# Optimization experiments

Hardware: AMD Instinct MI355X
Metric: run time of the kernel (lower is better)

Reference implementation:

```python
import jax, jax.numpy as jnp
import numpy as np


def _layernorm(x, g, b, eps=1e-5):
    m = x.mean(-1, keepdims=True)
    v = ((x - m) ** 2).mean(-1, keepdims=True)
    return (x - m) / jnp.sqrt(v + eps) * g + b


def _rotate_every_two(x):
    x1 = x[..., ::2]
    x2 = x[..., 1::2]
    return jnp.stack([-x2, x1], axis=-1).reshape(x.shape)


def _segsum(x):
    # x: (..., L) of negative decay rates -> (..., L, L) bidirectional segment sums
    cs = jnp.cumsum(x, axis=-1)
    d = cs[..., :, None] - cs[..., None, :]
    L = x.shape[-1]
    i = jnp.arange(L)[:, None]
    j = jnp.arange(L)[None, :]
    # lower-tri (incl diag): cs[i]-cs[j]; strict upper: cs[j]-cs[i]; diag is 0
    return jnp.where(i >= j, d, -d)


def _forward(x, y, th, dw1_w, dw1_b, dw2_w, dw2_b, qw, qb, kw, kb, vw, vb,
             lepe_w, lepe_b, dt_w, dt_bias, A_log, ow, ob,
             n1_g, n1_b, ffn_w1, ffn_b1, ffn_w2, ffn_b2, n2_g, n2_b):
    B, C, H, W = x.shape
    nh = dt_bias.shape[0]
    hd = C // nh
    scaling = hd ** (-0.5)

    # dynamic gated fusion of the two kv branches (1x1 convs == channel matmuls)
    fusion = jnp.concatenate([y, th], axis=1)                      # (B,2C,H,W)
    hid = jax.nn.relu(jnp.einsum('bchw,oc->bohw', fusion, dw1_w) + dw1_b[None, :, None, None])
    logits = jnp.einsum('bchw,oc->bohw', hid, dw2_w) + dw2_b[None, :, None, None]
    wts = jax.nn.softmax(logits, axis=1)                           # (B,2,H,W)
    fused = y * wts[:, 0:1] + th * wts[:, 1:2]

    xh = jnp.transpose(x, (0, 2, 3, 1))                            # (B,H,W,C)
    fkv = jnp.transpose(fused, (0, 2, 3, 1))

    # 2D RoPE tables (flattened raster index)
    angle = jnp.repeat(1.0 / 10000 ** jnp.linspace(0.0, 1.0, hd // 2), 2)
    idx = jnp.arange(H * W, dtype=x.dtype)
    sin = jnp.sin(idx[:, None] * angle[None, :]).reshape(H, W, hd)
    cos = jnp.cos(idx[:, None] * angle[None, :]).reshape(H, W, hd)

    q = xh @ qw + qb
    k = fkv @ kw + kb
    v = fkv @ vw + vb

    # depthwise 5x5 conv position term on v (NHWC)
    lepe = jax.lax.conv_general_dilated(
        v, lepe_w, (1, 1), ((2, 2), (2, 2)),
        dimension_numbers=('NHWC', 'HWIO', 'NHWC'), feature_group_count=C) + lepe_b

    k = k * scaling
    q = q.reshape(B, H, W, nh, hd).transpose(0, 3, 1, 2, 4)        # (B,nh,H,W,hd)
    k = k.reshape(B, H, W, nh, hd).transpose(0, 3, 1, 2, 4)
    v5 = v.reshape(B, H, W, nh, hd).transpose(0, 3, 1, 2, 4)

    qr = q * cos + _rotate_every_two(q) * sin
    kr = k * cos + _rotate_every_two(k) * sin

    # PathEmbeding2D: data-dependent decay masks
    xt = xh.reshape(B, H * W, nh, hd)
    dt = xt @ dt_w                                                 # (B,S,nh,2)
    A = -jnp.exp(A_log)                                            # (nh,)
    da = jax.nn.softplus(dt[..., 0] + dt_bias) * A                 # (B,S,nh)
    db = jax.nn.softplus(dt[..., 1] + dt_bias) * A
    mask_w = _segsum(da.reshape(B, H, W, nh).transpose(0, 1, 3, 2))  # (B,H,nh,W,W)
    mask_h = _segsum(db.reshape(B, H, W, nh).transpose(0, 2, 3, 1))  # (B,W,nh,H,H)

    # row (width-direction) and column (height-direction) attentions
    qk_w = jax.nn.softmax(jnp.einsum('bnhid,bnhjd->bhnij', qr, kr) + mask_w, axis=-1)  # (B,H,nh,W,W)
    qk_h = jax.nn.softmax(jnp.einsum('bnhwd,bngwd->bwnhg', qr, kr) + mask_h, axis=-1)  # (B,W,nh,H,H)

    v_w = jnp.einsum('bhnij,bnhjd->bhnid', qk_w, v5)               # (B,H,nh,W,hd)
    out1 = jnp.einsum('bwnhg,bgnwd->bwnhd', qk_h, v_w)             # (B,W,nh,H,hd)
    out1 = out1.transpose(0, 3, 1, 2, 4).reshape(B, H, W, C)

    v_h = jnp.einsum('bwnhg,bngwd->bwnhd', qk_h, v5)               # (B,W,nh,H,hd)
    out2 = jnp.einsum('bhnij,bjnhd->bhnid', qk_w, v_h)             # (B,H,nh,W,hd)
    out2 = out2.transpose(0, 1, 3, 2, 4).reshape(B, H, W, C)

    out = 0.5 * out1 + 0.5 * out2 + lepe
    out = out @ ow + ob
    out = _layernorm(xh + out, n1_g, n1_b)
    ffn = jax.nn.gelu(out @ ffn_w1 + ffn_b1, approximate=False) @ ffn_w2 + ffn_b2
    out = _layernorm(out + ffn, n2_g, n2_b)
    return jnp.transpose(out, (0, 3, 1, 2))                        # (B,C,H,W)


def setup_inputs() -> dict:
    B, C, H, W, nh = 4, 64, 128, 128, 4
    hd = C // nh
    key = jax.random.key(0)
    ks = jax.random.split(key, 20)
    n = lambda k, shp, s: jax.random.normal(k, shp, dtype=jnp.float32) * s
    rng = np.random.default_rng(0)
    dt = np.exp(rng.uniform(0.0, 1.0, nh) * (np.log(0.1) - np.log(0.001)) + np.log(0.001))
    dt = np.clip(dt, 1e-4, None)
    dt_bias = jnp.asarray(dt + np.log(-np.expm1(-dt)), dtype=jnp.float32)
    A_log = jnp.asarray(np.log(rng.uniform(1.0, 1.1, nh)), dtype=jnp.float32)
    inp = {
        'x': n(ks[0], (B, C, H, W), 1.0),
        'y': n(ks[1], (B, C, H, W), 1.0),
        'th': n(ks[2], (B, C, H, W), 1.0),
        'dw1_w': n(ks[3], (C, 2 * C), (2 * C) ** -0.5),
        'dw1_b': jnp.zeros((C,), jnp.float32),
        'dw2_w': n(ks[4], (2, C), C ** -0.5),
        'dw2_b': jnp.zeros((2,), jnp.float32),
        'qw': n(ks[5], (C, C), 0.2 * C ** -0.5),
        'qb': jnp.zeros((C,), jnp.float32),
        'kw': n(ks[6], (C, C), 0.2 * C ** -0.5),
        'kb': jnp.zeros((C,), jnp.float32),
        'vw': n(ks[7], (C, C), 0.2 * C ** -0.5),
        'vb': jnp.zeros((C,), jnp.float32),
        'lepe_w': n(ks[8], (5, 5, 1, C), 0.1),
        'lepe_b': jnp.zeros((C,), jnp.float32),
        'dt_w': n(ks[9], (hd, 2), hd ** -0.5),
        'dt_bias': dt_bias,
        'A_log': A_log,
        'ow': n(ks[10], (C, C), C ** -0.5),
        'ob': jnp.zeros((C,), jnp.float32),
        'n1_g': jnp.ones((C,), jnp.float32),
        'n1_b': jnp.zeros((C,), jnp.float32),
        'ffn_w1': n(ks[11], (C, 4 * C), C ** -0.5),
        'ffn_b1': jnp.zeros((4 * C,), jnp.float32),
        'ffn_w2': n(ks[12], (4 * C, C), (4 * C) ** -0.5),
        'ffn_b2': jnp.zeros((C,), jnp.float32),
        'n2_g': jnp.ones((C,), jnp.float32),
        'n2_b': jnp.zeros((C,), jnp.float32),
    }
    return inp


def reference(x, y, th, dw1_w, dw1_b, dw2_w, dw2_b, qw, qb, kw, kb, vw, vb,
              lepe_w, lepe_b, dt_w, dt_bias, A_log, ow, ob,
              n1_g, n1_b, ffn_w1, ffn_b1, ffn_w2, ffn_b2, n2_g, n2_b):
    return _forward(x, y, th, dw1_w, dw1_b, dw2_w, dw2_b, qw, qb, kw, kb, vw, vb,
                    lepe_w, lepe_b, dt_w, dt_bias, A_log, ow, ob,
                    n1_g, n1_b, ffn_w1, ffn_b1, ffn_w2, ffn_b2, n2_g, n2_b)
```

## Files before the change

### kernel.cpp

```cpp
#include <hip/hip_runtime.h>
#include <math.h>

#define HWSZ 16384

typedef __attribute__((ext_vector_type(8))) short bf16x8;
typedef __attribute__((ext_vector_type(4))) float f32x4;

__device__ __forceinline__ float gelu_f(float v) {
    return 0.5f * v * (1.0f + erff(v * 0.70710678118654752f));
}
__device__ __forceinline__ float splus_f(float v) {
    return (v > 20.f) ? v : log1pf(expf(v));
}
__device__ __forceinline__ unsigned short f2bf(float f) {
    union { float f; unsigned u; } v; v.f = f;
    unsigned r = (v.u + 0x7FFF + ((v.u >> 16) & 1)) >> 16;
    return (unsigned short)r;
}
__device__ __forceinline__ unsigned pk2(float a, float b) {
    return (unsigned)f2bf(a) | ((unsigned)f2bf(b) << 16);
}
__device__ __forceinline__ float bf2f(unsigned short s) {
    union { unsigned u; float f; } v; v.u = ((unsigned)s) << 16; return v.f;
}

#define W1S 68
__global__ __launch_bounds__(256) void k_fuse(
    const float* __restrict__ y, const float* __restrict__ th,
    const float* __restrict__ w1, const float* __restrict__ b1,
    const float* __restrict__ w2, const float* __restrict__ b2,
    float* __restrict__ fused)
{
    __shared__ unsigned short fsh[8192];
    __shared__ float w1t[128*W1S];
    int tid = threadIdx.x;
    int g = blockIdx.x;
    int b = g >> 8;
    int p0 = (g & 255)*64;
    for (int i = tid; i < 8192; i += 256) {
        int o = i >> 7, c = i & 127;
        w1t[c*W1S + o] = w1[i];
    }
    for (int vi = tid; vi < 1024; vi += 256) {
        int c = vi >> 4, p4 = (vi & 15)*4;
        float4 yv = *(const float4*)&y [((size_t)(b*64+c))*HWSZ + p0 + p4];
        float4 tv = *(const float4*)&th[((size_t)(b*64+c))*HWSZ + p0 + p4];
        *(uint2*)&fsh[c*64 + p4]      = make_uint2(pk2(yv.x,yv.y), pk2(yv.z,yv.w));
        *(uint2*)&fsh[(64+c)*64 + p4] = make_uint2(pk2(tv.x,tv.y), pk2(tv.z,tv.w));
    }
    __syncthreads();
    int lane = tid & 63, wv = tid >> 6;
    int po = lane & 15, oc = lane >> 4;
    int pos = wv*16 + po;
    float acc[16];
    #pragma unroll
    for (int d4 = 0; d4 < 4; ++d4) {
        float4 bv = *(const float4*)&b1[oc*16 + d4*4];
        acc[d4*4+0]=bv.x; acc[d4*4+1]=bv.y; acc[d4*4+2]=bv.z; acc[d4*4+3]=bv.w;
    }
    for (int c = 0; c < 128; ++c) {
        float xc = bf2f(fsh[c*64 + pos]);
        #pragma unroll
        for (int d4 = 0; d4 < 4; ++d4) {
            float4 wv4 = *(const float4*)&w1t[c*W1S + oc*16 + d4*4];
            acc[d4*4+0] += wv4.x*xc; acc[d4*4+1] += wv4.y*xc;
            acc[d4*4+2] += wv4.z*xc; acc[d4*4+3] += wv4.w*xc;
        }
    }
    float l0 = 0.f, l1 = 0.f;
    #pragma unroll
    for (int d4 = 0; d4 < 4; ++d4) {
        float4 wa4 = *(const float4*)&w2[oc*16 + d4*4];
        float4 wb4 = *(const float4*)&w2[64 + oc*16 + d4*4];
        float h0 = fmaxf(acc[d4*4+0],0.f), h1 = fmaxf(acc[d4*4+1],0.f);
        float h2 = fmaxf(acc[d4*4+2],0.f), h3 = fmaxf(acc[d4*4+3],0.f);
        l0 += wa4.x*h0 + wa4.y*h1 + wa4.z*h2 + wa4.w*h3;
        l1 += wb4.x*h0 + wb4.y*h1 + wb4.z*h2 + wb4.w*h3;
    }
    l0 += __shfl_xor(l0, 16, 64); l0 += __shfl_xor(l0, 32, 64);
    l1 += __shfl_xor(l1, 16, 64); l1 += __shfl_xor(l1, 32, 64);
    l0 += b2[0]; l1 += b2[1];
    float m = fmaxf(l0, l1);
    float e0 = __expf(l0 - m), e1 = __expf(l1 - m);
    float inv = 1.f/(e0 + e1);
    float wa = e0*inv, wb = e1*inv;
    float* fb = fused + (size_t)b*64*HWSZ + p0 + pos;
    #pragma unroll
    for (int u = 0; u < 16; ++u) {
        int c = oc*16 + u;
        float fv = bf2f(fsh[c*64 + pos])*wa + bf2f(fsh[(64+c)*64 + pos])*wb;
        fb[(size_t)c*HWSZ] = fv;
    }
}

__global__ __launch_bounds__(256) void k_qkv(
    const float* __restrict__ x, const float* __restrict__ fused,
    const float* __restrict__ qw, const float* __restrict__ qb,
    const float* __restrict__ kw, const float* __restrict__ kb,
    const float* __restrict__ vw, const float* __restrict__ vb,
    const float* __restrict__ dtw, const float* __restrict__ dtb,
    const float* __restrict__ alog,
    float* __restrict__ qr, float* __restrict__ kr, float* __restrict__ v5,
    float* __restrict__ da, float* __restrict__ db)
{
    __shared__ float sw[12288];
    __shared__ float sx[4096];
    int tid = threadIdx.x;
    for (int i = tid*4; i < 4096; i += 1024) {
        *(float4*)&sw[i]      = *(const float4*)&qw[i];
        *(float4*)&sw[4096+i] = *(const float4*)&kw[i];
        *(float4*)&sw[8192+i] = *(const float4*)&vw[i];
    }
    int b  = blockIdx.x >> 8;
    int p0 = (blockIdx.x & 255)*64;
    for (int vi = tid; vi < 1024; vi += 256) {
        int c = vi >> 4, p4 = (vi & 15)*4;
        *(float4*)&sx[c*64 + p4] = *(const float4*)&x[((size_t)(b*64+c))*HWSZ + p0 + p4];
    }
    __syncthreads();
    int lane = tid & 63;
    int n = tid >> 6;
    int p = p0 + lane;
    int h = p >> 7, w = p & 127;
    float sn[8], cn[8];
    #pragma unroll
    for (int t = 0; t < 8; ++t) {
        float ang = exp2f(-1.89824462565f * (float)t);
        sincosf((float)p * ang, &sn[t], &cn[t]);
    }
    float a[16];
    #pragma unroll
    for (int d = 0; d < 16; ++d) a[d] = qb[n*16+d];
    for (int c = 0; c < 64; ++c) {
        float xc = sx[c*64 + lane];
        #pragma unroll
        for (int d4 = 0; d4 < 4; ++d4) {
            float4 wv = *(const float4*)&sw[c*64 + n*16 + d4*4];
            a[d4*4+0] += wv.x*xc; a[d4*4+1] += wv.y*xc;
            a[d4*4+2] += wv.z*xc; a[d4*4+3] += wv.w*xc;
        }
    }
    {
        float r[16];
        #pragma unroll
        for (int t = 0; t < 8; ++t) {
            r[2*t]   = a[2*t]*cn[t]   - a[2*t+1]*sn[t];
            r[2*t+1] = a[2*t+1]*cn[t] + a[2*t]*sn[t];
        }
        float* dst = qr + (((size_t)(b*4+n))*HWSZ + p)*16;
        #pragma unroll
        for (int d4 = 0; d4 < 4; ++d4)
            *(float4*)&dst[d4*4] = make_float4(r[d4*4],r[d4*4+1],r[d4*4+2],r[d4*4+3]);
    }
    {
        float dt0 = 0.f, dt1 = 0.f;
        #pragma unroll
        for (int d = 0; d < 16; ++d) {
            float xv = sx[(n*16+d)*64 + lane];
            dt0 += xv*dtw[2*d];
            dt1 += xv*dtw[2*d+1];
        }
        float A  = -expf(alog[n]);
        float bb = dtb[n];
        da[((b*128+h)*4+n)*128 + w] = splus_f(dt0+bb)*A;
        db[((b*128+w)*4+n)*128 + h] = splus_f(dt1+bb)*A;
    }
    __syncthreads();
    for (int vi = tid; vi < 1024; vi += 256) {
        int c = vi >> 4, p4 = (vi & 15)*4;
        *(float4*)&sx[c*64 + p4] = *(const float4*)&fused[((size_t)(b*64+c))*HWSZ + p0 + p4];
    }
    __syncthreads();
    #pragma unroll
    for (int d = 0; d < 16; ++d) a[d] = kb[n*16+d];
    for (int c = 0; c < 64; ++c) {
        float xc = sx[c*64 + lane];
        #pragma unroll
        for (int d4 = 0; d4 < 4; ++d4) {
            float4 wv = *(const float4*)&sw[4096 + c*64 + n*16 + d4*4];
            a[d4*4+0] += wv.x*xc; a[d4*4+1] += wv.y*xc;
            a[d4*4+2] += wv.z*xc; a[d4*4+3] += wv.w*xc;
        }
    }
    {
        float r[16];
        #pragma unroll
        for (int t = 0; t < 8; ++t) {
            float e = a[2*t]*0.25f, o = a[2*t+1]*0.25f;
            r[2*t]   = e*cn[t] - o*sn[t];
            r[2*t+1] = o*cn[t] + e*sn[t];
        }
        float* dst = kr + (((size_t)(b*4+n))*HWSZ + p)*16;
        #pragma unroll
        for (int d4 = 0; d4 < 4; ++d4)
            *(float4*)&dst[d4*4] = make_float4(r[d4*4],r[d4*4+1],r[d4*4+2],r[d4*4+3]);
    }
    #pragma unroll
    for (int d = 0; d < 16; ++d) a[d] = vb[n*16+d];
    for (int c = 0; c < 64; ++c) {
        float xc = sx[c*64 + lane];
        #pragma unroll
        for (int d4 = 0; d4 < 4; ++d4) {
            float4 wv = *(const float4*)&sw[8192 + c*64 + n*16 + d4*4];
            a[d4*4+0] += wv.x*xc; a[d4*4+1] += wv.y*xc;
            a[d4*4+2] += wv.z*xc; a[d4*4+3] += wv.w*xc;
        }
    }
    {
        float* dst = v5 + (((size_t)(b*4+n))*HWSZ + p)*16;
        #pragma unroll
        for (int d4 = 0; d4 < 4; ++d4)
            *(float4*)&dst[d4*4] = make_float4(a[d4*4],a[d4*4+1],a[d4*4+2],a[d4*4+3]);
    }
}

__global__ __launch_bounds__(256) void k_cumsum(float* __restrict__ da, float* __restrict__ db)
{
    int gw = (blockIdx.x*256 + threadIdx.x) >> 6;
    int lane = threadIdx.x & 63;
    float* base = (gw < 2048) ? (da + (size_t)gw*128) : (db + (size_t)(gw-2048)*128);
    float2 e = *(float2*)&base[lane*2];
    float s = e.x + e.y;
    #pragma unroll
    for (int d = 1; d < 64; d <<= 1) {
        float t = __shfl_up(s, d, 64);
        if (lane >= d) s += t;
    }
    float excl = s - (e.x + e.y);
    float2 o;
    o.x = excl + e.x;
    o.y = excl + e.x + e.y;
    *(float2*)&base[lane*2] = o;
}

#define LROW 328
__global__ __launch_bounds__(256) void k_lepe(
    const float* __restrict__ v5, const float* __restrict__ lw,
    const float* __restrict__ lb, float* __restrict__ lepe)
{
    __shared__ float sv[36*LROW];
    __shared__ float swt[400];
    int tid = threadIdx.x, bid = blockIdx.x;
    int tw = bid & 7, th_ = (bid >> 3) & 3, n = (bid >> 5) & 3, b = bid >> 7;
    int bn = b*4 + n;
    int h0 = th_*32, w0 = tw*16;
    for (int i = tid; i < 400; i += 256) {
        int tap = i >> 4, d = i & 15;
        swt[i] = lw[tap*64 + n*16 + d];
    }
    const float* vb = v5 + (size_t)bn*HWSZ*16;
    for (int vi = tid; vi < 2880; vi += 256) {
        int hh = vi / 80;
        int rem = vi - hh*80;
        int ww = rem >> 2, df = (rem & 3)*4;
        int h = h0 - 2 + hh, w = w0 - 2 + ww;
        float4 val = make_float4(0.f,0.f,0.f,0.f);
        if (h >= 0 && h < 128 && w >= 0 && w < 128)
            val = *(const float4*)&vb[((size_t)(h*128+w))*16 + df];
        *(float4*)&sv[hh*LROW + ww*16 + df] = val;
    }
    __syncthreads();
    int df = (tid & 3)*4;
    int s  = tid >> 2;
    int ph = s >> 1;
    int pw = (s & 1)*8;
    float4 bv = *(const float4*)&lb[n*16 + df];
    float acc[8][4];
    #pragma unroll
    for (int ow = 0; ow < 8; ++ow) {
        acc[ow][0] = bv.x; acc[ow][1] = bv.y; acc[ow][2] = bv.z; acc[ow][3] = bv.w;
    }
    #pragma unroll
    for (int ky = 0; ky < 5; ++ky) {
        float wgt[5][4];
        #pragma unroll
        for (int kx = 0; kx < 5; ++kx) {
            float4 wv = *(const float4*)&swt[(ky*5+kx)*16 + df];
            wgt[kx][0]=wv.x; wgt[kx][1]=wv.y; wgt[kx][2]=wv.z; wgt[kx][3]=wv.w;
        }
        float dat[13][4];
        #pragma unroll
        for (int c = 0; c < 13; ++c) {
            float4 dv = *(const float4*)&sv[(ph+ky)*LROW + (pw+c)*16 + df];
            dat[c][0]=dv.x; dat[c][1]=dv.y; dat[c][2]=dv.z; dat[c][3]=dv.w;
        }
        #pragma unroll
        for (int ow = 0; ow < 8; ++ow)
            #pragma unroll
            for (int kx = 0; kx < 5; ++kx)
                #pragma unroll
                for (int u = 0; u < 4; ++u)
                    acc[ow][u] += dat[ow+kx][u]*wgt[kx][u];
    }
    float* ob = lepe + ((size_t)bn*HWSZ + (size_t)(h0+ph)*128 + w0+pw)*16 + df;
    #pragma unroll
    for (int ow = 0; ow < 8; ++ow)
        *(float4*)&ob[ow*16] = make_float4(acc[ow][0],acc[ow][1],acc[ow][2],acc[ow][3]);
}

__global__ __launch_bounds__(256) void k_attn_w1(
    const float* __restrict__ qr, const float* __restrict__ kr,
    const float* __restrict__ v5, const float* __restrict__ dacs,
    float* __restrict__ vwb)
{
    __shared__ unsigned short Qs[128*40], Ks[128*40], Vt[16*136], Ps[128*136];
    __shared__ float csr[128], linv[128];
    int tid = threadIdx.x, bid = blockIdx.x;
    int h = bid & 127, n = (bid >> 7) & 3, b = bid >> 9;
    size_t rowoff = ((size_t)((b*4+n)*128 + h)) * 2048;
    {
        int i = tid >> 1, seg = (tid & 1)*8;
        *(uint4*)&Qs[i*40 + 16 + seg] = make_uint4(0,0,0,0);
        *(uint4*)&Ks[i*40 + 16 + seg] = make_uint4(0,0,0,0);
    }
    for (int vi = tid; vi < 512; vi += 256) {
        int i = vi >> 2, d4 = (vi & 3)*4;
        float4 q = *(const float4*)&qr[rowoff + i*16 + d4];
        float4 k = *(const float4*)&kr[rowoff + i*16 + d4];
        *(uint2*)&Qs[i*40 + d4] = make_uint2(pk2(q.x,q.y), pk2(q.z,q.w));
        *(uint2*)&Ks[i*40 + d4] = make_uint2(pk2(k.x,k.y), pk2(k.z,k.w));
    }
    {
        int jp = tid >> 2, d4 = (tid & 3)*4;
        float4 a = *(const float4*)&v5[rowoff + (2*jp)*16 + d4];
        float4 c = *(const float4*)&v5[rowoff + (2*jp+1)*16 + d4];
        *(unsigned*)&Vt[(d4+0)*136 + 2*jp] = pk2(a.x, c.x);
        *(unsigned*)&Vt[(d4+1)*136 + 2*jp] = pk2(a.y, c.y);
        *(unsigned*)&Vt[(d4+2)*136 + 2*jp] = pk2(a.z, c.z);
        *(unsigned*)&Vt[(d4+3)*136 + 2*jp] = pk2(a.w, c.w);
    }
    if (tid < 128) csr[tid] = dacs[((b*128+h)*4+n)*128 + tid];
    __syncthreads();
    int lane = tid & 63, wv = tid >> 6;
    int quad = lane >> 4, lm = lane & 15;
    int r0 = wv*32, r1 = wv*32 + 16;
    bf16x8 aQ0 = *(bf16x8*)&Qs[(r0+lm)*40 + quad*8];
    bf16x8 aQ1 = *(bf16x8*)&Qs[(r1+lm)*40 + quad*8];
    float csj[8], csi0[4], csi1[4];
    #pragma unroll
    for (int jt = 0; jt < 8; ++jt) csj[jt] = csr[jt*16+lm];
    #pragma unroll
    for (int r = 0; r < 4; ++r) { csi0[r] = csr[r0+quad*4+r]; csi1[r] = csr[r1+quad*4+r]; }
    float ls0[4]={0,0,0,0}, ls1[4]={0,0,0,0};
    f32x4 z = {0.f,0.f,0.f,0.f};
    #pragma unroll
    for (int jt = 0; jt < 8; ++jt) {
        bf16x8 bK = *(bf16x8*)&Ks[(jt*16+lm)*40 + quad*8];
        f32x4 s0 = __builtin_amdgcn_mfma_f32_16x16x32_bf16(aQ0, bK, z, 0,0,0);
        f32x4 s1 = __builtin_amdgcn_mfma_f32_16x16x32_bf16(aQ1, bK, z, 0,0,0);
        #pragma unroll
        for (int r = 0; r < 4; ++r) {
            float e0 = __expf(s0[r] - fabsf(csi0[r]-csj[jt])); ls0[r] += e0;
            float e1 = __expf(s1[r] - fabsf(csi1[r]-csj[jt])); ls1[r] += e1;
            Ps[(r0+quad*4+r)*136 + jt*16+lm] = f2bf(e0);
            Ps[(r1+quad*4+r)*136 + jt*16+lm] = f2bf(e1);
        }
    }
    #pragma unroll
    for (int r = 0; r < 4; ++r) {
        #pragma unroll
        for (int m = 1; m < 16; m <<= 1) {
            ls0[r] += __shfl_xor(ls0[r], m, 64);
            ls1[r] += __shfl_xor(ls1[r], m, 64);
        }
        if (lm == 0) { linv[r0+quad*4+r] = 1.f/ls0[r]; linv[r1+quad*4+r] = 1.f/ls1[r]; }
    }
    __syncthreads();
    f32x4 acc0 = z, acc1 = z;
    #pragma unroll
    for (int c = 0; c < 4; ++c) {
        bf16x8 bV  = *(bf16x8*)&Vt[lm*136 + c*32 + quad*8];
        bf16x8 aP0 = *(bf16x8*)&Ps[(r0+lm)*136 + c*32 + quad*8];
        bf16x8 aP1 = *(bf16x8*)&Ps[(r1+lm)*136 + c*32 + quad*8];
        acc0 = __builtin_amdgcn_mfma_f32_16x16x32_bf16(aP0, bV, acc0, 0,0,0);
        acc1 = __builtin_amdgcn_mfma_f32_16x16x32_bf16(aP1, bV, acc1, 0,0,0);
    }
    #pragma unroll
    for (int r = 0; r < 4; ++r) {
        int i0 = r0+quad*4+r, i1 = r1+quad*4+r;
        vwb[rowoff + (size_t)i0*16 + lm] = acc0[r]*linv[i0];
        vwb[rowoff + (size_t)i1*16 + lm] = acc1[r]*linv[i1];
    }
}

__global__ __launch_bounds__(256) void k_attn_h(
    const float* __restrict__ qr, const float* __restrict__ kr,
    const float* __restrict__ v5, const float* __restrict__ vwb,
    const float* __restrict__ dbcs,
    float* __restrict__ vhb, float* __restrict__ o1b)
{
    __shared__ unsigned short Qs[128*40], Ks[128*40], Vt[16*136], Wt[16*136], Ps[128*136];
    __shared__ float csr[128], linv[128];
    int tid = threadIdx.x, bid = blockIdx.x;
    int w = bid & 127, n = (bid >> 7) & 3, b = bid >> 9;
    int bn = b*4 + n;
    size_t base = ((size_t)bn*16384 + w)*16;
    {
        int i = tid >> 1, seg = (tid & 1)*8;
        *(uint4*)&Qs[i*40 + 16 + seg] = make_uint4(0,0,0,0);
        *(uint4*)&Ks[i*40 + 16 + seg] = make_uint4(0,0,0,0);
    }
    for (int vi = tid; vi < 512; vi += 256) {
        int i = vi >> 2, d4 = (vi & 3)*4;
        float4 q = *(const float4*)&qr[base + (size_t)i*2048 + d4];
        float4 k = *(const float4*)&kr[base + (size_t)i*2048 + d4];
        *(uint2*)&Qs[i*40 + d4] = make_uint2(pk2(q.x,q.y), pk2(q.z,q.w));
        *(uint2*)&Ks[i*40 + d4] = make_uint2(pk2(k.x,k.y), pk2(k.z,k.w));
    }
    {
        int jp = tid >> 2, d4 = (tid & 3)*4;
        float4 a = *(const float4*)&v5[base + (size_t)(2*jp)*2048 + d4];
        float4 c = *(const float4*)&v5[base + (size_t)(2*jp+1)*2048 + d4];
        *(unsigned*)&Vt[(d4+0)*136 + 2*jp] = pk2(a.x, c.x);
        *(unsigned*)&Vt[(d4+1)*136 + 2*jp] = pk2(a.y, c.y);
        *(unsigned*)&Vt[(d4+2)*136 + 2*jp] = pk2(a.z, c.z);
        *(unsigned*)&Vt[(d4+3)*136 + 2*jp] = pk2(a.w, c.w);
        float4 e = *(const float4*)&vwb[base + (size_t)(2*jp)*2048 + d4];
        float4 f = *(const float4*)&vwb[base + (size_t)(2*jp+1)*2048 + d4];
        *(unsigned*)&Wt[(d4+0)*136 + 2*jp] = pk2(e.x, f.x);
        *(unsigned*)&Wt[(d4+1)*136 + 2*jp] = pk2(e.y, f.y);
        *(unsigned*)&Wt[(d4+2)*136 + 2*jp] = pk2(e.z, f.z);
        *(unsigned*)&Wt[(d4+3)*136 + 2*jp] = pk2(e.w, f.w);
    }
    if (tid < 128) csr[tid] = dbcs[((b*128+w)*4+n)*128 + tid];
    __syncthreads();
    int lane = tid & 63, wv = tid >> 6;
    int quad = lane >> 4, lm = lane & 15;
    int r0 = wv*32, r1 = wv*32 + 16;
    bf16x8 aQ0 = *(bf16x8*)&Qs[(r0+lm)*40 + quad*8];
    bf16x8 aQ1 = *(bf16x8*)&Qs[(r1+lm)*40 + quad*8];
    float csj[8], csi0[4], csi1[4];
    #pragma unroll
    for (int jt = 0; jt < 8; ++jt) csj[jt] = csr[jt*16+lm];
    #pragma unroll
    for (int r = 0; r < 4; ++r) { csi0[r] = csr[r0+quad*4+r]; csi1[r] = csr[r1+quad*4+r]; }
    float ls0[4]={0,0,0,0}, ls1[4]={0,0,0,0};
    f32x4 z = {0.f,0.f,0.f,0.f};
    #pragma unroll
    for (int jt = 0; jt < 8; ++jt) {
        bf16x8 bK = *(bf16x8*)&Ks[(jt*16+lm)*40 + quad*8];
        f32x4 s0 = __builtin_amdgcn_mfma_f32_16x16x32_bf16(aQ0, bK, z, 0,0,0);
        f32x4 s1 = __builtin_amdgcn_mfma_f32_16x16x32_bf16(aQ1, bK, z, 0,0,0);
        #pragma unroll
        for (int r = 0; r < 4; ++r) {
            float e0 = __expf(s0[r] - fabsf(csi0[r]-csj[jt])); ls0[r] += e0;
            float e1 = __expf(s1[r] - fabsf(csi1[r]-csj[jt])); ls1[r] += e1;
            Ps[(r0+quad*4+r)*136 + jt*16+lm] = f2bf(e0);
            Ps[(r1+quad*4+r)*136 + jt*16+lm] = f2bf(e1);
        }
    }
    #pragma unroll
    for (int r = 0; r < 4; ++r) {
        #pragma unroll
        for (int m = 1; m < 16; m <<= 1) {
            ls0[r] += __shfl_xor(ls0[r], m, 64);
            ls1[r] += __shfl_xor(ls1[r], m, 64);
        }
        if (lm == 0) { linv[r0+quad*4+r] = 1.f/ls0[r]; linv[r1+quad*4+r] = 1.f/ls1[r]; }
    }
    __syncthreads();
    f32x4 aV0 = z, aV1 = z, aW0 = z, aW1 = z;
    #pragma unroll
    for (int c = 0; c < 4; ++c) {
        bf16x8 bV  = *(bf16x8*)&Vt[lm*136 + c*32 + quad*8];
        bf16x8 bW  = *(bf16x8*)&Wt[lm*136 + c*32 + quad*8];
        bf16x8 aP0 = *(bf16x8*)&Ps[(r0+lm)*136 + c*32 + quad*8];
        bf16x8 aP1 = *(bf16x8*)&Ps[(r1+lm)*136 + c*32 + quad*8];
        aV0 = __builtin_amdgcn_mfma_f32_16x16x32_bf16(aP0, bV, aV0, 0,0,0);
        aV1 = __builtin_amdgcn_mfma_f32_16x16x32_bf16(aP1, bV, aV1, 0,0,0);
        aW0 = __builtin_amdgcn_mfma_f32_16x16x32_bf16(aP0, bW, aW0, 0,0,0);
        aW1 = __builtin_amdgcn_mfma_f32_16x16x32_bf16(aP1, bW, aW1, 0,0,0);
    }
    size_t obase = ((size_t)bn*16384 + (size_t)w*128)*16;
    #pragma unroll
    for (int r = 0; r < 4; ++r) {
        int i0 = r0+quad*4+r, i1 = r1+quad*4+r;
        float v0 = linv[i0], v1 = linv[i1];
        vhb[obase + (size_t)i0*16 + lm] = aV0[r]*v0;
        vhb[obase + (size_t)i1*16 + lm] = aV1[r]*v1;
        o1b[obase + (size_t)i0*16 + lm] = aW0[r]*v0;
        o1b[obase + (size_t)i1*16 + lm] = aW1[r]*v1;
    }
}

__global__ __launch_bounds__(256) void k_attn_w2(
    const float* __restrict__ qr, const float* __restrict__ kr,
    const float* __restrict__ vhb, const float* __restrict__ o1b,
    const float* __restrict__ dacs, const float* __restrict__ lepe,
    float* __restrict__ attn)
{
    __shared__ unsigned short Qs[128*40], Ks[128*40], Vt[16*136], Ps[128*136];
    __shared__ float csr[128], linv[128];
    int tid = threadIdx.x, bid = blockIdx.x;
    int h = bid & 127, n = (bid >> 7) & 3, b = bid >> 9;
    int bn = b*4 + n;
    size_t rowoff = ((size_t)(bn*128 + h)) * 2048;
    size_t vbase  = (size_t)bn*262144 + (size_t)h*16;
    {
        int i = tid >> 1, seg = (tid & 1)*8;
        *(uint4*)&Qs[i*40 + 16 + seg] = make_uint4(0,0,0,0);
        *(uint4*)&Ks[i*40 + 16 + seg] = make_uint4(0,0,0,0);
    }
    for (int vi = tid; vi < 512; vi += 256) {
        int i = vi >> 2, d4 = (vi & 3)*4;
        float4 q = *(const float4*)&qr[rowoff + i*16 + d4];
        float4 k = *(const float4*)&kr[rowoff + i*16 + d4];
        *(uint2*)&Qs[i*40 + d4] = make_uint2(pk2(q.x,q.y), pk2(q.z,q.w));
        *(uint2*)&Ks[i*40 + d4] = make_uint2(pk2(k.x,k.y), pk2(k.z,k.w));
    }
    {
        int jp = tid >> 2, d4 = (tid & 3)*4;
        float4 a = *(const float4*)&vhb[vbase + (size_t)(2*jp)*2048 + d4];
        float4 c = *(const float4*)&vhb[vbase + (size_t)(2*jp+1)*2048 + d4];
        *(unsigned*)&Vt[(d4+0)*136 + 2*jp] = pk2(a.x, c.x);
        *(unsigned*)&Vt[(d4+1)*136 + 2*jp] = pk2(a.y, c.y);
        *(unsigned*)&Vt[(d4+2)*136 + 2*jp] = pk2(a.z, c.z);
        *(unsigned*)&Vt[(d4+3)*136 + 2*jp] = pk2(a.w, c.w);
    }
    if (tid < 128) csr[tid] = dacs[((b*128+h)*4+n)*128 + tid];
    __syncthreads();
    int lane = tid & 63, wv = tid >> 6;
    int quad = lane >> 4, lm = lane & 15;
    int r0 = wv*32, r1 = wv*32 + 16;
    bf16x8 aQ0 = *(bf16x8*)&Qs[(r0+lm)*40 + quad*8];
    bf16x8 aQ1 = *(bf16x8*)&Qs[(r1+lm)*40 + quad*8];
    float csj[8], csi0[4], csi1[4];
    #pragma unroll
    for (int jt = 0; jt < 8; ++jt) csj[jt] = csr[jt*16+lm];
    #pragma unroll
    for (int r = 0; r < 4; ++r) { csi0[r] = csr[r0+quad*4+r]; csi1[r] = csr[r1+quad*4+r]; }
    float ls0[4]={0,0,0,0}, ls1[4]={0,0,0,0};
    f32x4 z = {0.f,0.f,0.f,0.f};
    #pragma unroll
    for (int jt = 0; jt < 8; ++jt) {
        bf16x8 bK = *(bf16x8*)&Ks[(jt*16+lm)*40 + quad*8];
        f32x4 s0 = __builtin_amdgcn_mfma_f32_16x16x32_bf16(aQ0, bK, z, 0,0,0);
        f32x4 s1 = __builtin_amdgcn_mfma_f32_16x16x32_bf16(aQ1, bK, z, 0,0,0);
        #pragma unroll
        for (int r = 0; r < 4; ++r) {
            float e0 = __expf(s0[r] - fabsf(csi0[r]-csj[jt])); ls0[r] += e0;
            float e1 = __expf(s1[r] - fabsf(csi1[r]-csj[jt])); ls1[r] += e1;
            Ps[(r0+quad*4+r)*136 + jt*16+lm] = f2bf(e0);
            Ps[(r1+quad*4+r)*136 + jt*16+lm] = f2bf(e1);
        }
    }
    #pragma unroll
    for (int r = 0; r < 4; ++r) {
        #pragma unroll
        for (int m = 1; m < 16; m <<= 1) {
            ls0[r] += __shfl_xor(ls0[r], m, 64);
            ls1[r] += __shfl_xor(ls1[r], m, 64);
        }
        if (lm == 0) { linv[r0+quad*4+r] = 1.f/ls0[r]; linv[r1+quad*4+r] = 1.f/ls1[r]; }
    }
    __syncthreads();
    f32x4 acc0 = z, acc1 = z;
    #pragma unroll
    for (int c = 0; c < 4; ++c) {
        bf16x8 bV  = *(bf16x8*)&Vt[lm*136 + c*32 + quad*8];
        bf16x8 aP0 = *(bf16x8*)&Ps[(r0+lm)*136 + c*32 + quad*8];
        bf16x8 aP1 = *(bf16x8*)&Ps[(r1+lm)*136 + c*32 + quad*8];
        acc0 = __builtin_amdgcn_mfma_f32_16x16x32_bf16(aP0, bV, acc0, 0,0,0);
        acc1 = __builtin_amdgcn_mfma_f32_16x16x32_bf16(aP1, bV, acc1, 0,0,0);
    }
    size_t lpb = (size_t)bn*262144 + (size_t)h*2048;
    size_t oab = (size_t)b*1048576 + (size_t)h*8192 + n*16;
    #pragma unroll
    for (int r = 0; r < 4; ++r) {
        int i0 = r0+quad*4+r, i1 = r1+quad*4+r;
        float o2a = acc0[r]*linv[i0];
        float o2b = acc1[r]*linv[i1];
        float o1a = o1b[vbase + (size_t)i0*2048 + lm];
        float o1c = o1b[vbase + (size_t)i1*2048 + lm];
        float la  = lepe[lpb + (size_t)i0*16 + lm];
        float lc  = lepe[lpb + (size_t)i1*16 + lm];
        attn[oab + (size_t)i0*64 + lm] = 0.5f*(o1a + o2a) + la;
        attn[oab + (size_t)i1*64 + lm] = 0.5f*(o1c + o2b) + lc;
    }
}

__global__ __launch_bounds__(256) void k_proj_ln(
    const float* __restrict__ attn, const float* __restrict__ x,
    const float* __restrict__ ow, const float* __restrict__ ob,
    const float* __restrict__ g1, const float* __restrict__ b1,
    float* __restrict__ t1)
{
    __shared__ unsigned short As[128*72];
    __shared__ unsigned short Bs[64*72];
    __shared__ float XT[8704];
    int tid = threadIdx.x, bid = blockIdx.x;
    int pbase = bid*128;
    int b = pbase >> 14, p0 = pbase & 16383;
    for (int vi = tid; vi < 2048; vi += 256) {
        int p = vi >> 4, c4 = (vi & 15)*4;
        float4 v = *(const float4*)&attn[((size_t)(pbase+p))*64 + c4];
        *(uint2*)&As[p*72 + c4] = make_uint2(pk2(v.x,v.y), pk2(v.z,v.w));
    }
    for (int vi = tid; vi < 512; vi += 256) {
        int kp = vi >> 4, c4 = (vi & 15)*4;
        float4 a = *(const float4*)&ow[(2*kp)*64 + c4];
        float4 c = *(const float4*)&ow[(2*kp+1)*64 + c4];
        *(unsigned*)&Bs[(c4+0)*72 + 2*kp] = pk2(a.x, c.x);
        *(unsigned*)&Bs[(c4+1)*72 + 2*kp] = pk2(a.y, c.y);
        *(unsigned*)&Bs[(c4+2)*72 + 2*kp] = pk2(a.z, c.z);
        *(unsigned*)&Bs[(c4+3)*72 + 2*kp] = pk2(a.w, c.w);
    }
    for (int vi = tid; vi < 2048; vi += 256) {
        int c = vi >> 5, p4 = (vi & 31)*4;
        *(float4*)&XT[c*132 + p4] = *(const float4*)&x[((size_t)(b*64+c))*HWSZ + p0 + p4];
    }
    __syncthreads();
    int lane = tid & 63, wv = tid >> 6;
    int quad = lane >> 4, lm = lane & 15;
    int M0 = wv*32;
    float xv[2][4][4], obv[4], g1v[4], b1v[4];
    #pragma unroll
    for (int nt = 0; nt < 4; ++nt) {
        int c = nt*16 + lm;
        obv[nt] = ob[c]; g1v[nt] = g1[c]; b1v[nt] = b1[c];
        #pragma unroll
        for (int mt = 0; mt < 2; ++mt)
            #pragma unroll
            for (int r = 0; r < 4; ++r)
                xv[mt][nt][r] = XT[c*132 + M0 + mt*16 + quad*4 + r];
    }
    f32x4 z = {0.f,0.f,0.f,0.f};
    f32x4 acc[2][4];
    #pragma unroll
    for (int mt = 0; mt < 2; ++mt)
        #pragma unroll
        for (int nt = 0; nt < 4; ++nt) acc[mt][nt] = z;
    #pragma unroll
    for (int ks = 0; ks < 2; ++ks) {
        bf16x8 aF[2];
        #pragma unroll
        for (int mt = 0; mt < 2; ++mt)
            aF[mt] = *(bf16x8*)&As[(M0+mt*16+lm)*72 + ks*32 + quad*8];
        #pragma unroll
        for (int nt = 0; nt < 4; ++nt) {
            bf16x8 bF = *(bf16x8*)&Bs[(nt*16+lm)*72 + ks*32 + quad*8];
            #pragma unroll
            for (int mt = 0; mt < 2; ++mt)
                acc[mt][nt] = __builtin_amdgcn_mfma_f32_16x16x32_bf16(aF[mt], bF, acc[mt][nt], 0,0,0);
        }
    }
    float val[2][4][4], res[2][4][4];
    #pragma unroll
    for (int mt = 0; mt < 2; ++mt) {
        #pragma unroll
        for (int r = 0; r < 4; ++r) {
            float s = 0.f;
            #pragma unroll
            for (int nt = 0; nt < 4; ++nt) {
                val[mt][nt][r] = acc[mt][nt][r] + obv[nt] + xv[mt][nt][r];
                s += val[mt][nt][r];
            }
            s += __shfl_xor(s, 1, 64); s += __shfl_xor(s, 2, 64);
            s += __shfl_xor(s, 4, 64); s += __shfl_xor(s, 8, 64);
            float mean = s*(1.f/64.f);
            float vv = 0.f;
            #pragma unroll
            for (int nt = 0; nt < 4; ++nt) {
                float d = val[mt][nt][r] - mean;
                vv += d*d;
            }
            vv += __shfl_xor(vv, 1, 64); vv += __shfl_xor(vv, 2, 64);
            vv += __shfl_xor(vv, 4, 64); vv += __shfl_xor(vv, 8, 64);
            float rs = rsqrtf(vv*(1.f/64.f) + 1e-5f);
            #pragma unroll
            for (int nt = 0; nt < 4; ++nt)
                res[mt][nt][r] = (val[mt][nt][r] - mean)*rs*g1v[nt] + b1v[nt];
        }
    }
    __syncthreads();
    float* outT = XT;
    #pragma unroll
    for (int mt = 0; mt < 2; ++mt)
        #pragma unroll
        for (int r = 0; r < 4; ++r)
            #pragma unroll
            for (int nt = 0; nt < 4; ++nt)
                outT[(M0+mt*16+quad*4+r)*68 + nt*16 + lm] = res[mt][nt][r];
    __syncthreads();
    for (int vi = tid; vi < 2048; vi += 256) {
        int p = vi >> 4, c4 = (vi & 15)*4;
        *(float4*)&t1[((size_t)(pbase+p))*64 + c4] = *(const float4*)&outT[p*68 + c4];
    }
}

__global__ __launch_bounds__(256) void k_ffn(
    const float* __restrict__ t1, const float* __restrict__ w1,
    const float* __restrict__ b1f, const float* __restrict__ w2,
    const float* __restrict__ b2f, const float* __restrict__ g2,
    const float* __restrict__ bb2, float* __restrict__ outp)
{
    __shared__ unsigned short At1[128*72];
    __shared__ unsigned short WH[2*64*72 + 128*72];
    __shared__ float sb1[256];
    __shared__ float sb2[64], sg[64], sbb[64];
    unsigned short* W1b = WH;
    unsigned short* W2b = WH + 4608;
    unsigned short* Hid = WH + 9216;
    int tid = threadIdx.x, bid = blockIdx.x;
    int pbase = bid*128;
    int b = pbase >> 14, p0 = pbase & 16383;
    for (int vi = tid; vi < 2048; vi += 256) {
        int p = vi >> 4, c4 = (vi & 15)*4;
        float4 v = *(const float4*)&t1[((size_t)(pbase+p))*64 + c4];
        *(uint2*)&At1[p*72 + c4] = make_uint2(pk2(v.x,v.y), pk2(v.z,v.w));
    }
    if (tid < 256) sb1[tid] = b1f[tid];
    if (tid < 64) { sb2[tid] = b2f[tid]; sg[tid] = g2[tid]; sbb[tid] = bb2[tid]; }
    int lane = tid & 63, wv = tid >> 6;
    int quad = lane >> 4, lm = lane & 15;
    int M0 = wv*32;
    f32x4 z = {0.f,0.f,0.f,0.f};
    f32x4 acc2[2][4];
    #pragma unroll
    for (int mt = 0; mt < 2; ++mt)
        #pragma unroll
        for (int nt = 0; nt < 4; ++nt) acc2[mt][nt] = z;
    for (int jc = 0; jc < 4; ++jc) {
        __syncthreads();
        for (int vi = tid; vi < 512; vi += 256) {
            int kp = vi >> 4, c4 = (vi & 15)*4;
            float4 a = *(const float4*)&w1[(2*kp)*256 + jc*64 + c4];
            float4 c = *(const float4*)&w1[(2*kp+1)*256 + jc*64 + c4];
            *(unsigned*)&W1b[(c4+0)*72 + 2*kp] = pk2(a.x, c.x);
            *(unsigned*)&W1b[(c4+1)*72 + 2*kp] = pk2(a.y, c.y);
            *(unsigned*)&W1b[(c4+2)*72 + 2*kp] = pk2(a.z, c.z);
            *(unsigned*)&W1b[(c4+3)*72 + 2*kp] = pk2(a.w, c.w);
        }
        for (int vi = tid; vi < 512; vi += 256) {
            int kp = vi >> 4, c4 = (vi & 15)*4;
            float4 a = *(const float4*)&w2[(size_t)(jc*64 + 2*kp)*64 + c4];
            float4 c = *(const float4*)&w2[(size_t)(jc*64 + 2*kp+1)*64 + c4];
            *(unsigned*)&W2b[(c4+0)*72 + 2*kp] = pk2(a.x, c.x);
            *(unsigned*)&W2b[(c4+1)*72 + 2*kp] = pk2(a.y, c.y);
            *(unsigned*)&W2b[(c4+2)*72 + 2*kp] = pk2(a.z, c.z);
            *(unsigned*)&W2b[(c4+3)*72 + 2*kp] = pk2(a.w, c.w);
        }
        __syncthreads();
        f32x4 h[2][4];
        #pragma unroll
        for (int mt = 0; mt < 2; ++mt)
            #pragma unroll
            for (int nt = 0; nt < 4; ++nt) h[mt][nt] = z;
        #pragma unroll
        for (int ks = 0; ks < 2; ++ks) {
            bf16x8 aF[2];
            #pragma unroll
            for (int mt = 0; mt < 2; ++mt)
                aF[mt] = *(bf16x8*)&At1[(M0+mt*16+lm)*72 + ks*32 + quad*8];
            #pragma unroll
            for (int nt = 0; nt < 4; ++nt) {
                bf16x8 bF = *(bf16x8*)&W1b[(nt*16+lm)*72 + ks*32 + quad*8];
                #pragma unroll
                for (int mt = 0; mt < 2; ++mt)
                    h[mt][nt] = __builtin_amdgcn_mfma_f32_16x16x32_bf16(aF[mt], bF, h[mt][nt], 0,0,0);
            }
        }
        #pragma unroll
        for (int nt = 0; nt < 4; ++nt) {
            float bb = sb1[jc*64 + nt*16 + lm];
            #pragma unroll
            for (int mt = 0; mt < 2; ++mt)
                #pragma unroll
                for (int r = 0; r < 4; ++r) {
                    float hv = gelu_f(h[mt][nt][r] + bb);
                    unsigned u = (unsigned)f2bf(hv);
                    unsigned up = (unsigned)__shfl_xor((int)u, 1, 64);
                    if (!(lm & 1))
                        *(unsigned*)&Hid[(M0+mt*16+quad*4+r)*72 + nt*16 + lm] = (u & 0xffff) | (up << 16);
                }
        }
        #pragma unroll
        for (int ks = 0; ks < 2; ++ks) {
            bf16x8 aH[2];
            #pragma unroll
            for (int mt = 0; mt < 2; ++mt)
                aH[mt] = *(bf16x8*)&Hid[(M0+mt*16+lm)*72 + ks*32 + quad*8];
            #pragma unroll
            for (int nt = 0; nt < 4; ++nt) {
                bf16x8 bF = *(bf16x8*)&W2b[(nt*16+lm)*72 + ks*32 + quad*8];
                #pragma unroll
                for (int mt = 0; mt < 2; ++mt)
                    acc2[mt][nt] = __builtin_amdgcn_mfma_f32_16x16x32_bf16(aH[mt], bF, acc2[mt][nt], 0,0,0);
            }
        }
    }
    float val[2][4][4], res[2][4][4];
    float sb2v[4], sgv[4], sbbv[4];
    #pragma unroll
    for (int nt = 0; nt < 4; ++nt) {
        int c = nt*16 + lm;
        sb2v[nt] = sb2[c]; sgv[nt] = sg[c]; sbbv[nt] = sbb[c];
    }
    #pragma unroll
    for (int mt = 0; mt < 2; ++mt) {
        #pragma unroll
        for (int r = 0; r < 4; ++r) {
            int pos = M0 + mt*16 + quad*4 + r;
            float s = 0.f;
            #pragma unroll
            for (int nt = 0; nt < 4; ++nt) {
                float tv = bf2f(At1[pos*72 + nt*16 + lm]);
                val[mt][nt][r] = acc2[mt][nt][r] + sb2v[nt] + tv;
                s += val[mt][nt][r];
            }
            s += __shfl_xor(s, 1, 64); s += __shfl_xor(s, 2, 64);
            s += __shfl_xor(s, 4, 64); s += __shfl_xor(s, 8, 64);
            float mean = s*(1.f/64.f);
            float vv = 0.f;
            #pragma unroll
            for (int nt = 0; nt < 4; ++nt) {
                float d = val[mt][nt][r] - mean;
                vv += d*d;
            }
            vv += __shfl_xor(vv, 1, 64); vv += __shfl_xor(vv, 2, 64);
            vv += __shfl_xor(vv, 4, 64); vv += __shfl_xor(vv, 8, 64);
            float rs = rsqrtf(vv*(1.f/64.f) + 1e-5f);
            #pragma unroll
            for (int nt = 0; nt < 4; ++nt)
                res[mt][nt][r] = (val[mt][nt][r] - mean)*rs*sgv[nt] + sbbv[nt];
        }
    }
    __syncthreads();
    float* outT = (float*)WH;
    #pragma unroll
    for (int mt = 0; mt < 2; ++mt)
        #pragma unroll
        for (int r = 0; r < 4; ++r)
            #pragma unroll
            for (int nt = 0; nt < 4; ++nt)
                outT[(nt*16+lm)*132 + M0 + mt*16 + quad*4 + r] = res[mt][nt][r];
    __syncthreads();
    for (int vi = tid; vi < 2048; vi += 256) {
        int c = vi >> 5, p4 = (vi & 31)*4;
        *(float4*)&outp[((size_t)(b*64+c))*HWSZ + p0 + p4] = *(const float4*)&outT[c*132 + p4];
    }
}

extern "C" void kernel_launch(void* const* d_in, const int* in_sizes, int n_in,
                              void* d_out, int out_size, void* d_ws, size_t ws_size,
                              hipStream_t stream) {
    const float* x      = (const float*)d_in[0];
    const float* y      = (const float*)d_in[1];
    const float* th     = (const float*)d_in[2];
    const float* dw1_w  = (const float*)d_in[3];
    const float* dw1_b  = (const float*)d_in[4];
    const float* dw2_w  = (const float*)d_in[5];
    const float* dw2_b  = (const float*)d_in[6];
    const float* qw     = (const float*)d_in[7];
    const float* qb     = (const float*)d_in[8];
    const float* kw     = (const float*)d_in[9];
    const float* kb     = (const float*)d_in[10];
    const float* vw     = (const float*)d_in[11];
    const float* vb     = (const float*)d_in[12];
    const float* lepe_w = (const float*)d_in[13];
    const float* lepe_b = (const float*)d_in[14];
    const float* dt_w   = (const float*)d_in[15];
    const float* dt_bias= (const float*)d_in[16];
    const float* A_log  = (const float*)d_in[17];
    const float* ow     = (const float*)d_in[18];
    const float* ob     = (const float*)d_in[19];
    const float* n1_g   = (const float*)d_in[20];
    const float* n1_b   = (const float*)d_in[21];
    const float* ffn_w1 = (const float*)d_in[22];
    const float* ffn_b1 = (const float*)d_in[23];
    const float* ffn_w2 = (const float*)d_in[24];
    const float* ffn_b2 = (const float*)d_in[25];
    const float* n2_g   = (const float*)d_in[26];
    const float* n2_b   = (const float*)d_in[27];
    float* out = (float*)d_out;

    const size_t SZ = 4194304;
    float* ws    = (float*)d_ws;
    float* fused = ws + 0*SZ;
    float* qrb   = ws + 1*SZ;
    float* krb   = ws + 2*SZ;
    float* v5b   = ws + 3*SZ;
    float* lepeb = ws + 4*SZ;
    float* vhb   = ws + 5*SZ;
    float* o1b   = ws + 6*SZ;
    float* attnb = ws + 7*SZ;
    float* t1b   = ws + 8*SZ;
    float* dacs  = ws + 9*SZ;
    float* dbcs  = ws + 9*SZ + 262144;

    k_fuse<<<1024, 256, 0, stream>>>(y, th, dw1_w, dw1_b, dw2_w, dw2_b, fused);
    k_qkv<<<1024, 256, 0, stream>>>(x, fused, qw, qb, kw, kb, vw, vb,
                                    dt_w, dt_bias, A_log, qrb, krb, v5b, dacs, dbcs);
    k_cumsum<<<1024, 256, 0, stream>>>(dacs, dbcs);
    k_lepe<<<512, 256, 0, stream>>>(v5b, lepe_w, lepe_b, lepeb);
    k_attn_w1<<<2048, 256, 0, stream>>>(qrb, krb, v5b, dacs, fused);
    k_attn_h<<<2048, 256, 0, stream>>>(qrb, krb, v5b, fused, dbcs, vhb, o1b);
    k_attn_w2<<<2048, 256, 0, stream>>>(qrb, krb, vhb, o1b, dacs, lepeb, attnb);
    k_proj_ln<<<512, 256, 0, stream>>>(attnb, x, ow, ob, n1_g, n1_b, t1b);
    k_ffn<<<512, 256, 0, stream>>>(t1b, ffn_w1, ffn_b1, ffn_w2, ffn_b2, n2_g, n2_b, out);
}
```

Baseline: 354.3 us.

## Store intermediates in bf16 and move QKV projection to MFMA

```diff
diff --git a/kernel.cpp b/kernel.cpp
--- a/kernel.cpp
+++ b/kernel.cpp
@@ -5,6 +5,10 @@
 
 typedef __attribute__((ext_vector_type(8))) short bf16x8;
 typedef __attribute__((ext_vector_type(4))) float f32x4;
+typedef unsigned short u16;
+
+union U4 { uint4 v; u16 s[8]; };
+union U2 { uint2 v; u16 s[4]; };
 
 __device__ __forceinline__ float gelu_f(float v) {
     return 0.5f * v * (1.0f + erff(v * 0.70710678118654752f));
@@ -12,15 +16,15 @@
 __device__ __forceinline__ float splus_f(float v) {
     return (v > 20.f) ? v : log1pf(expf(v));
 }
-__device__ __forceinline__ unsigned short f2bf(float f) {
+__device__ __forceinline__ u16 f2bf(float f) {
     union { float f; unsigned u; } v; v.f = f;
     unsigned r = (v.u + 0x7FFF + ((v.u >> 16) & 1)) >> 16;
-    return (unsigned short)r;
+    return (u16)r;
 }
 __device__ __forceinline__ unsigned pk2(float a, float b) {
     return (unsigned)f2bf(a) | ((unsigned)f2bf(b) << 16);
 }
-__device__ __forceinline__ float bf2f(unsigned short s) {
+__device__ __forceinline__ float bf2f(u16 s) {
     union { unsigned u; float f; } v; v.u = ((unsigned)s) << 16; return v.f;
 }
 
@@ -29,9 +33,9 @@
     const float* __restrict__ y, const float* __restrict__ th,
     const float* __restrict__ w1, const float* __restrict__ b1,
     const float* __restrict__ w2, const float* __restrict__ b2,
-    float* __restrict__ fused)
+    u16* __restrict__ fused)
 {
-    __shared__ unsigned short fsh[8192];
+    __shared__ u16 fsh[8192];
     __shared__ float w1t[128*W1S];
     int tid = threadIdx.x;
     int g = blockIdx.x;
@@ -84,133 +88,145 @@
     float e0 = __expf(l0 - m), e1 = __expf(l1 - m);
     float inv = 1.f/(e0 + e1);
     float wa = e0*inv, wb = e1*inv;
-    float* fb = fused + (size_t)b*64*HWSZ + p0 + pos;
+    u16* fb = fused + (size_t)b*64*HWSZ + p0 + pos;
     #pragma unroll
     for (int u = 0; u < 16; ++u) {
         int c = oc*16 + u;
         float fv = bf2f(fsh[c*64 + pos])*wa + bf2f(fsh[(64+c)*64 + pos])*wb;
-        fb[(size_t)c*HWSZ] = fv;
+        fb[(size_t)c*HWSZ] = f2bf(fv);
     }
 }
 
 __global__ __launch_bounds__(256) void k_qkv(
-    const float* __restrict__ x, const float* __restrict__ fused,
+    const float* __restrict__ x, const u16* __restrict__ fused,
     const float* __restrict__ qw, const float* __restrict__ qb,
     const float* __restrict__ kw, const float* __restrict__ kb,
     const float* __restrict__ vw, const float* __restrict__ vb,
     const float* __restrict__ dtw, const float* __restrict__ dtb,
     const float* __restrict__ alog,
-    float* __restrict__ qr, float* __restrict__ kr, float* __restrict__ v5,
+    u16* __restrict__ qr, u16* __restrict__ kr, u16* __restrict__ v5,
     float* __restrict__ da, float* __restrict__ db)
 {
-    __shared__ float sw[12288];
-    __shared__ float sx[4096];
-    int tid = threadIdx.x;
-    for (int i = tid*4; i < 4096; i += 1024) {
-        *(float4*)&sw[i]      = *(const float4*)&qw[i];
-        *(float4*)&sw[4096+i] = *(const float4*)&kw[i];
-        *(float4*)&sw[8192+i] = *(const float4*)&vw[i];
-    }
-    int b  = blockIdx.x >> 8;
-    int p0 = (blockIdx.x & 255)*64;
+    __shared__ u16 Ax[128*72];
+    __shared__ u16 Af[128*72];
+    __shared__ u16 Bq[64*72], Bk[64*72], Bv[64*72];
+    int tid = threadIdx.x, bid = blockIdx.x;
+    int pbase = bid*128;
+    int b = pbase >> 14, p0 = pbase & 16383;
+    for (int vi = tid; vi < 2048; vi += 256) {
+        int c = vi >> 5, pg = (vi & 31)*4;
+        float4 xv = *(const float4*)&x[((size_t)(b*64+c))*HWSZ + p0 + pg];
+        Ax[(pg+0)*72 + c] = f2bf(xv.x);
+        Ax[(pg+1)*72 + c] = f2bf(xv.y);
+        Ax[(pg+2)*72 + c] = f2bf(xv.z);
+        Ax[(pg+3)*72 + c] = f2bf(xv.w);
+    }
     for (int vi = tid; vi < 1024; vi += 256) {
-        int c = vi >> 4, p4 = (vi & 15)*4;
-        *(float4*)&sx[c*64 + p4] = *(const float4*)&x[((size_t)(b*64+c))*HWSZ + p0 + p4];
-    }
-    __syncthreads();
-    int lane = tid & 63;
-    int n = tid >> 6;
-    int p = p0 + lane;
-    int h = p >> 7, w = p & 127;
-    float sn[8], cn[8];
-    #pragma unroll
-    for (int t = 0; t < 8; ++t) {
-        float ang = exp2f(-1.89824462565f * (float)t);
-        sincosf((float)p * ang, &sn[t], &cn[t]);
-    }
-    float a[16];
-    #pragma unroll
-    for (int d = 0; d < 16; ++d) a[d] = qb[n*16+d];
-    for (int c = 0; c < 64; ++c) {
-        float xc = sx[c*64 + lane];
-        #pragma unroll
-        for (int d4 = 0; d4 < 4; ++d4) {
-            float4 wv = *(const float4*)&sw[c*64 + n*16 + d4*4];
-            a[d4*4+0] += wv.x*xc; a[d4*4+1] += wv.y*xc;
-            a[d4*4+2] += wv.z*xc; a[d4*4+3] += wv.w*xc;
+        int c = vi >> 4, pg = (vi & 15)*8;
+        U4 fv; fv.v = *(const uint4*)&fused[((size_t)(b*64+c))*HWSZ + p0 + pg];
+        #pragma unroll
+        for (int u = 0; u < 8; ++u) Af[(pg+u)*72 + c] = fv.s[u];
+    }
+    for (int vi = tid; vi < 1024; vi += 256) {
+        int c = vi >> 4, o4 = (vi & 15)*4;
+        float4 q = *(const float4*)&qw[c*64 + o4];
+        float4 k = *(const float4*)&kw[c*64 + o4];
+        float4 v = *(const float4*)&vw[c*64 + o4];
+        Bq[(o4+0)*72+c]=f2bf(q.x); Bq[(o4+1)*72+c]=f2bf(q.y); Bq[(o4+2)*72+c]=f2bf(q.z); Bq[(o4+3)*72+c]=f2bf(q.w);
+        Bk[(o4+0)*72+c]=f2bf(k.x); Bk[(o4+1)*72+c]=f2bf(k.y); Bk[(o4+2)*72+c]=f2bf(k.z); Bk[(o4+3)*72+c]=f2bf(k.w);
+        Bv[(o4+0)*72+c]=f2bf(v.x); Bv[(o4+1)*72+c]=f2bf(v.y); Bv[(o4+2)*72+c]=f2bf(v.z); Bv[(o4+3)*72+c]=f2bf(v.w);
+    }
+    __syncthreads();
+    int lane = tid & 63, wv = tid >> 6;
+    int quad = lane >> 4, lm = lane & 15;
+    int M0 = wv*32;
+    f32x4 z = {0.f,0.f,0.f,0.f};
+    f32x4 accQ[2][4], accK[2][4], accV[2][4];
+    #pragma unroll
+    for (int mt = 0; mt < 2; ++mt)
+        #pragma unroll
+        for (int nt = 0; nt < 4; ++nt) { accQ[mt][nt]=z; accK[mt][nt]=z; accV[mt][nt]=z; }
+    #pragma unroll
+    for (int ks = 0; ks < 2; ++ks) {
+        bf16x8 aX[2], aF[2];
+        #pragma unroll
+        for (int mt = 0; mt < 2; ++mt) {
+            aX[mt] = *(bf16x8*)&Ax[(M0+mt*16+lm)*72 + ks*32 + quad*8];
+            aF[mt] = *(bf16x8*)&Af[(M0+mt*16+lm)*72 + ks*32 + quad*8];
+        }
+        #pragma unroll
+        for (int nt = 0; nt < 4; ++nt) {
+            bf16x8 bQ = *(bf16x8*)&Bq[(nt*16+lm)*72 + ks*32 + quad*8];
+            bf16x8 bK = *(bf16x8*)&Bk[(nt*16+lm)*72 + ks*32 + quad*8];
+            bf16x8 bV = *(bf16x8*)&Bv[(nt*16+lm)*72 + ks*32 + quad*8];
+            #pragma unroll
+            for (int mt = 0; mt < 2; ++mt) {
+                accQ[mt][nt] = __builtin_amdgcn_mfma_f32_16x16x32_bf16(aX[mt], bQ, accQ[mt][nt], 0,0,0);
+                accK[mt][nt] = __builtin_amdgcn_mfma_f32_16x16x32_bf16(aF[mt], bK, accK[mt][nt], 0,0,0);
+                accV[mt][nt] = __builtin_amdgcn_mfma_f32_16x16x32_bf16(aF[mt], bV, accV[mt][nt], 0,0,0);
+            }
         }
     }
     {
-        float r[16];
-        #pragma unroll
-        for (int t = 0; t < 8; ++t) {
-            r[2*t]   = a[2*t]*cn[t]   - a[2*t+1]*sn[t];
-            r[2*t+1] = a[2*t+1]*cn[t] + a[2*t]*sn[t];
-        }
-        float* dst = qr + (((size_t)(b*4+n))*HWSZ + p)*16;
-        #pragma unroll
-        for (int d4 = 0; d4 < 4; ++d4)
-            *(float4*)&dst[d4*4] = make_float4(r[d4*4],r[d4*4+1],r[d4*4+2],r[d4*4+3]);
-    }
-    {
-        float dt0 = 0.f, dt1 = 0.f;
-        #pragma unroll
-        for (int d = 0; d < 16; ++d) {
-            float xv = sx[(n*16+d)*64 + lane];
-            dt0 += xv*dtw[2*d];
-            dt1 += xv*dtw[2*d+1];
-        }
-        float A  = -expf(alog[n]);
-        float bb = dtb[n];
-        da[((b*128+h)*4+n)*128 + w] = splus_f(dt0+bb)*A;
-        db[((b*128+w)*4+n)*128 + h] = splus_f(dt1+bb)*A;
-    }
-    __syncthreads();
-    for (int vi = tid; vi < 1024; vi += 256) {
-        int c = vi >> 4, p4 = (vi & 15)*4;
-        *(float4*)&sx[c*64 + p4] = *(const float4*)&fused[((size_t)(b*64+c))*HWSZ + p0 + p4];
-    }
-    __syncthreads();
-    #pragma unroll
-    for (int d = 0; d < 16; ++d) a[d] = kb[n*16+d];
-    for (int c = 0; c < 64; ++c) {
-        float xc = sx[c*64 + lane];
-        #pragma unroll
-        for (int d4 = 0; d4 < 4; ++d4) {
-            float4 wv = *(const float4*)&sw[4096 + c*64 + n*16 + d4*4];
-            a[d4*4+0] += wv.x*xc; a[d4*4+1] += wv.y*xc;
-            a[d4*4+2] += wv.z*xc; a[d4*4+3] += wv.w*xc;
-        }
-    }
-    {
-        float r[16];
-        #pragma unroll
-        for (int t = 0; t < 8; ++t) {
-            float e = a[2*t]*0.25f, o = a[2*t+1]*0.25f;
-            r[2*t]   = e*cn[t] - o*sn[t];
-            r[2*t+1] = o*cn[t] + e*sn[t];
-        }
-        float* dst = kr + (((size_t)(b*4+n))*HWSZ + p)*16;
-        #pragma unroll
-        for (int d4 = 0; d4 < 4; ++d4)
-            *(float4*)&dst[d4*4] = make_float4(r[d4*4],r[d4*4+1],r[d4*4+2],r[d4*4+3]);
-    }
-    #pragma unroll
-    for (int d = 0; d < 16; ++d) a[d] = vb[n*16+d];
-    for (int c = 0; c < 64; ++c) {
-        float xc = sx[c*64 + lane];
-        #pragma unroll
-        for (int d4 = 0; d4 < 4; ++d4) {
-            float4 wv = *(const float4*)&sw[8192 + c*64 + n*16 + d4*4];
-            a[d4*4+0] += wv.x*xc; a[d4*4+1] += wv.y*xc;
-            a[d4*4+2] += wv.z*xc; a[d4*4+3] += wv.w*xc;
-        }
-    }
-    {
-        float* dst = v5 + (((size_t)(b*4+n))*HWSZ + p)*16;
-        #pragma unroll
-        for (int d4 = 0; d4 < 4; ++d4)
-            *(float4*)&dst[d4*4] = make_float4(a[d4*4],a[d4*4+1],a[d4*4+2],a[d4*4+3]);
+        float dtw_[32];
+        #pragma unroll
+        for (int i = 0; i < 32; ++i) dtw_[i] = dtw[i];
+        #pragma unroll
+        for (int rep = 0; rep < 2; ++rep) {
+            int pair = tid + rep*256;
+            int p = pair >> 2, n = pair & 3;
+            float dt0 = 0.f, dt1 = 0.f;
+            #pragma unroll
+            for (int d = 0; d < 16; ++d) {
+                float xv = bf2f(Ax[p*72 + n*16 + d]);
+                dt0 += xv*dtw_[2*d];
+                dt1 += xv*dtw_[2*d+1];
+            }
+            float A = -expf(alog[n]);
+            float bb = dtb[n];
+            int P = p0 + p;
+            int h = P >> 7, w = P & 127;
+            da[((b*128+h)*4+n)*128 + w] = splus_f(dt0+bb)*A;
+            db[((b*128+w)*4+n)*128 + h] = splus_f(dt1+bb)*A;
+        }
+    }
+    float qbv[4], kbv[4], vbv[4];
+    #pragma unroll
+    for (int nt = 0; nt < 4; ++nt) {
+        qbv[nt] = qb[nt*16+lm]; kbv[nt] = kb[nt*16+lm]; vbv[nt] = vb[nt*16+lm];
+    }
+    bool evn = !(lm & 1);
+    float ang = exp2f(-1.89824462565f * (float)(lm >> 1));
+    int bb4 = b*4;
+    #pragma unroll
+    for (int mt = 0; mt < 2; ++mt) {
+        #pragma unroll
+        for (int r = 0; r < 4; ++r) {
+            int P = p0 + M0 + mt*16 + quad*4 + r;
+            float sn_, cs_;
+            sincosf((float)P * ang, &sn_, &cs_);
+            #pragma unroll
+            for (int nt = 0; nt < 4; ++nt) {
+                float vq = accQ[mt][nt][r] + qbv[nt];
+                float pq = __shfl_xor(vq, 1, 64);
+                float rq = evn ? vq*cs_ - pq*sn_ : vq*cs_ + pq*sn_;
+                unsigned uq = f2bf(rq);
+                unsigned upq = (unsigned)__shfl_xor((int)uq, 1, 64);
+                float vk = (accK[mt][nt][r] + kbv[nt])*0.25f;
+                float pk = __shfl_xor(vk, 1, 64);
+                float rk = evn ? vk*cs_ - pk*sn_ : vk*cs_ + pk*sn_;
+                unsigned uk = f2bf(rk);
+                unsigned upk = (unsigned)__shfl_xor((int)uk, 1, 64);
+                unsigned uv = f2bf(accV[mt][nt][r] + vbv[nt]);
+                unsigned upv = (unsigned)__shfl_xor((int)uv, 1, 64);
+                if (evn) {
+                    size_t off = ((size_t)(bb4+nt)*HWSZ + P)*16 + lm;
+                    *(unsigned*)&qr[off] = (uq & 0xffff) | (upq << 16);
+                    *(unsigned*)&kr[off] = (uk & 0xffff) | (upk << 16);
+                    *(unsigned*)&v5[off] = (uv & 0xffff) | (upv << 16);
+                }
+            }
+        }
     }
 }
 
@@ -235,7 +251,7 @@
 
 #define LROW 328
 __global__ __launch_bounds__(256) void k_lepe(
-    const float* __restrict__ v5, const float* __restrict__ lw,
+    const u16* __restrict__ v5, const float* __restrict__ lw,
     const float* __restrict__ lb, float* __restrict__ lepe)
 {
     __shared__ float sv[36*LROW];
@@ -248,16 +264,17 @@
         int tap = i >> 4, d = i & 15;
         swt[i] = lw[tap*64 + n*16 + d];
     }
-    const float* vb = v5 + (size_t)bn*HWSZ*16;
-    for (int vi = tid; vi < 2880; vi += 256) {
-        int hh = vi / 80;
-        int rem = vi - hh*80;
-        int ww = rem >> 2, df = (rem & 3)*4;
+    const u16* vb = v5 + (size_t)bn*HWSZ*16;
+    for (int vi = tid; vi < 1440; vi += 256) {
+        int cell = vi >> 1, half = vi & 1;
+        int hh = cell/20, ww = cell - hh*20;
         int h = h0 - 2 + hh, w = w0 - 2 + ww;
-        float4 val = make_float4(0.f,0.f,0.f,0.f);
+        U4 val; val.v = make_uint4(0,0,0,0);
         if (h >= 0 && h < 128 && w >= 0 && w < 128)
-            val = *(const float4*)&vb[((size_t)(h*128+w))*16 + df];
-        *(float4*)&sv[hh*LROW + ww*16 + df] = val;
+            val.v = *(const uint4*)&vb[((size_t)(h*128+w))*16 + half*8];
+        float* dst = &sv[hh*LROW + ww*16 + half*8];
+        #pragma unroll
+        for (int u = 0; u < 8; ++u) dst[u] = bf2f(val.s[u]);
     }
     __syncthreads();
     int df = (tid & 3)*4;
@@ -299,11 +316,11 @@
 }
 
 __global__ __launch_bounds__(256) void k_attn_w1(
-    const float* __restrict__ qr, const float* __restrict__ kr,
-    const float* __restrict__ v5, const float* __restrict__ dacs,
-    float* __restrict__ vwb)
+    const u16* __restrict__ qr, const u16* __restrict__ kr,
+    const u16* __restrict__ v5, const float* __restrict__ dacs,
+    u16* __restrict__ vwb)
 {
-    __shared__ unsigned short Qs[128*40], Ks[128*40], Vt[16*136], Ps[128*136];
+    __shared__ u16 Qs[128*40], Ks[128*40], Vt[16*136], Ps[128*136];
     __shared__ float csr[128], linv[128];
     int tid = threadIdx.x, bid = blockIdx.x;
     int h = bid & 127, n = (bid >> 7) & 3, b = bid >> 9;
@@ -313,21 +330,19 @@
         *(uint4*)&Qs[i*40 + 16 + seg] = make_uint4(0,0,0,0);
         *(uint4*)&Ks[i*40 + 16 + seg] = make_uint4(0,0,0,0);
     }
-    for (int vi = tid; vi < 512; vi += 256) {
-        int i = vi >> 2, d4 = (vi & 3)*4;
-        float4 q = *(const float4*)&qr[rowoff + i*16 + d4];
-        float4 k = *(const float4*)&kr[rowoff + i*16 + d4];
-        *(uint2*)&Qs[i*40 + d4] = make_uint2(pk2(q.x,q.y), pk2(q.z,q.w));
-        *(uint2*)&Ks[i*40 + d4] = make_uint2(pk2(k.x,k.y), pk2(k.z,k.w));
-    }
     {
-        int jp = tid >> 2, d4 = (tid & 3)*4;
-        float4 a = *(const float4*)&v5[rowoff + (2*jp)*16 + d4];
-        float4 c = *(const float4*)&v5[rowoff + (2*jp+1)*16 + d4];
-        *(unsigned*)&Vt[(d4+0)*136 + 2*jp] = pk2(a.x, c.x);
-        *(unsigned*)&Vt[(d4+1)*136 + 2*jp] = pk2(a.y, c.y);
-        *(unsigned*)&Vt[(d4+2)*136 + 2*jp] = pk2(a.z, c.z);
-        *(unsigned*)&Vt[(d4+3)*136 + 2*jp] = pk2(a.w, c.w);
+        int i = tid >> 1, half = tid & 1;
+        *(uint4*)&Qs[i*40 + half*8] = *(const uint4*)&qr[rowoff + i*16 + half*8];
+        *(uint4*)&Ks[i*40 + half*8] = *(const uint4*)&kr[rowoff + i*16 + half*8];
+    }
+    {
+        int jp = tid >> 2, q4 = tid & 3;
+        U2 a, c;
+        a.v = *(const uint2*)&v5[rowoff + (2*jp)*16 + q4*4];
+        c.v = *(const uint2*)&v5[rowoff + (2*jp+1)*16 + q4*4];
+        #pragma unroll
+        for (int u = 0; u < 4; ++u)
+            *(unsigned*)&Vt[(q4*4+u)*136 + 2*jp] = (unsigned)a.s[u] | ((unsigned)c.s[u] << 16);
     }
     if (tid < 128) csr[tid] = dacs[((b*128+h)*4+n)*128 + tid];
     __syncthreads();
@@ -375,21 +390,28 @@
         acc0 = __builtin_amdgcn_mfma_f32_16x16x32_bf16(aP0, bV, acc0, 0,0,0);
         acc1 = __builtin_amdgcn_mfma_f32_16x16x32_bf16(aP1, bV, acc1, 0,0,0);
     }
+    bool evn = !(lm & 1);
     #pragma unroll
     for (int r = 0; r < 4; ++r) {
         int i0 = r0+quad*4+r, i1 = r1+quad*4+r;
-        vwb[rowoff + (size_t)i0*16 + lm] = acc0[r]*linv[i0];
-        vwb[rowoff + (size_t)i1*16 + lm] = acc1[r]*linv[i1];
+        unsigned u0 = f2bf(acc0[r]*linv[i0]);
+        unsigned u1 = f2bf(acc1[r]*linv[i1]);
+        unsigned up0 = (unsigned)__shfl_xor((int)u0, 1, 64);
+        unsigned up1 = (unsigned)__shfl_xor((int)u1, 1, 64);
+        if (evn) {
+            *(unsigned*)&vwb[rowoff + (size_t)i0*16 + lm] = (u0 & 0xffff) | (up0 << 16);
+            *(unsigned*)&vwb[rowoff + (size_t)i1*16 + lm] = (u1 & 0xffff) | (up1 << 16);
+        }
     }
 }
 
 __global__ __launch_bounds__(256) void k_attn_h(
-    const float* __restrict__ qr, const float* __restrict__ kr,
-    const float* __restrict__ v5, const float* __restrict__ vwb,
+    const u16* __restrict__ qr, const u16* __restrict__ kr,
+    const u16* __restrict__ v5, const u16* __restrict__ vwb,
     const float* __restrict__ dbcs,
-    float* __restrict__ vhb, float* __restrict__ o1b)
+    u16* __restrict__ vhb, u16* __restrict__ o1b)
 {
-    __shared__ unsigned short Qs[128*40], Ks[128*40], Vt[16*136], Wt[16*136], Ps[128*136];
+    __shared__ u16 Qs[128*40], Ks[128*40], Vt[16*136], Wt[16*136], Ps[128*136];
     __shared__ float csr[128], linv[128];
     int tid = threadIdx.x, bid = blockIdx.x;
     int w = bid & 127, n = (bid >> 7) & 3, b = bid >> 9;
@@ -400,27 +422,23 @@
         *(uint4*)&Qs[i*40 + 16 + seg] = make_uint4(0,0,0,0);
         *(uint4*)&Ks[i*40 + 16 + seg] = make_uint4(0,0,0,0);
     }
-    for (int vi = tid; vi < 512; vi += 256) {
-        int i = vi >> 2, d4 = (vi & 3)*4;
-        float4 q = *(const float4*)&qr[base + (size_t)i*2048 + d4];
-        float4 k = *(const float4*)&kr[base + (size_t)i*2048 + d4];
-        *(uint2*)&Qs[i*40 + d4] = make_uint2(pk2(q.x,q.y), pk2(q.z,q.w));
-        *(uint2*)&Ks[i*40 + d4] = make_uint2(pk2(k.x,k.y), pk2(k.z,k.w));
-    }
     {
-        int jp = tid >> 2, d4 = (tid & 3)*4;
-        float4 a = *(const float4*)&v5[base + (size_t)(2*jp)*2048 + d4];
-        float4 c = *(const float4*)&v5[base + (size_t)(2*jp+1)*2048 + d4];
-        *(unsigned*)&Vt[(d4+0)*136 + 2*jp] = pk2(a.x, c.x);
-        *(unsigned*)&Vt[(d4+1)*136 + 2*jp] = pk2(a.y, c.y);
-        *(unsigned*)&Vt[(d4+2)*136 + 2*jp] = pk2(a.z, c.z);
-        *(unsigned*)&Vt[(d4+3)*136 + 2*jp] = pk2(a.w, c.w);
-        float4 e = *(const float4*)&vwb[base + (size_t)(2*jp)*2048 + d4];
-        float4 f = *(const float4*)&vwb[base + (size_t)(2*jp+1)*2048 + d4];
-        *(unsigned*)&Wt[(d4+0)*136 + 2*jp] = pk2(e.x, f.x);
-        *(unsigned*)&Wt[(d4+1)*136 + 2*jp] = pk2(e.y, f.y);
-        *(unsigned*)&Wt[(d4+2)*136 + 2*jp] = pk2(e.z, f.z);
-        *(unsigned*)&Wt[(d4+3)*136 + 2*jp] = pk2(e.w, f.w);
+        int i = tid >> 1, half = tid & 1;
+        *(uint4*)&Qs[i*40 + half*8] = *(const uint4*)&qr[base + (size_t)i*2048 + half*8];
+        *(uint4*)&Ks[i*40 + half*8] = *(const uint4*)&kr[base + (size_t)i*2048 + half*8];
+    }
+    {
+        int jp = tid >> 2, q4 = tid & 3;
+        U2 a, c, e, f;
+        a.v = *(const uint2*)&v5 [base + (size_t)(2*jp)*2048 + q4*4];
+        c.v = *(const uint2*)&v5 [base + (size_t)(2*jp+1)*2048 + q4*4];
+        e.v = *(const uint2*)&vwb[base + (size_t)(2*jp)*2048 + q4*4];
+        f.v = *(const uint2*)&vwb[base + (size_t)(2*jp+1)*2048 + q4*4];
+        #pragma unroll
+        for (int u = 0; u < 4; ++u) {
+            *(unsigned*)&Vt[(q4*4+u)*136 + 2*jp] = (unsigned)a.s[u] | ((unsigned)c.s[u] << 16);
+            *(unsigned*)&Wt[(q4*4+u)*136 + 2*jp] = (unsigned)e.s[u] | ((unsigned)f.s[u] << 16);
+        }
     }
     if (tid < 128) csr[tid] = dbcs[((b*128+w)*4+n)*128 + tid];
     __syncthreads();
@@ -472,24 +490,31 @@
         aW1 = __builtin_amdgcn_mfma_f32_16x16x32_bf16(aP1, bW, aW1, 0,0,0);
     }
     size_t obase = ((size_t)bn*16384 + (size_t)w*128)*16;
+    bool evn = !(lm & 1);
     #pragma unroll
     for (int r = 0; r < 4; ++r) {
         int i0 = r0+quad*4+r, i1 = r1+quad*4+r;
         float v0 = linv[i0], v1 = linv[i1];
-        vhb[obase + (size_t)i0*16 + lm] = aV0[r]*v0;
-        vhb[obase + (size_t)i1*16 + lm] = aV1[r]*v1;
-        o1b[obase + (size_t)i0*16 + lm] = aW0[r]*v0;
-        o1b[obase + (size_t)i1*16 + lm] = aW1[r]*v1;
+        unsigned a0 = f2bf(aV0[r]*v0), a1 = f2bf(aV1[r]*v1);
+        unsigned b0 = f2bf(aW0[r]*v0), b1 = f2bf(aW1[r]*v1);
+        unsigned ap0 = (unsigned)__shfl_xor((int)a0,1,64), ap1 = (unsigned)__shfl_xor((int)a1,1,64);
+        unsigned bp0 = (unsigned)__shfl_xor((int)b0,1,64), bp1 = (unsigned)__shfl_xor((int)b1,1,64);
+        if (evn) {
+            *(unsigned*)&vhb[obase + (size_t)i0*16 + lm] = (a0 & 0xffff) | (ap0 << 16);
+            *(unsigned*)&vhb[obase + (size_t)i1*16 + lm] = (a1 & 0xffff) | (ap1 << 16);
+            *(unsigned*)&o1b[obase + (size_t)i0*16 + lm] = (b0 & 0xffff) | (bp0 << 16);
+            *(unsigned*)&o1b[obase + (size_t)i1*16 + lm] = (b1 & 0xffff) | (bp1 << 16);
+        }
     }
 }
 
 __global__ __launch_bounds__(256) void k_attn_w2(
-    const float* __restrict__ qr, const float* __restrict__ kr,
-    const float* __restrict__ vhb, const float* __restrict__ o1b,
+    const u16* __restrict__ qr, const u16* __restrict__ kr,
+    const u16* __restrict__ vhb, const u16* __restrict__ o1b,
     const float* __restrict__ dacs, const float* __restrict__ lepe,
-    float* __restrict__ attn)
+    u16* __restrict__ attn)
 {
-    __shared__ unsigned short Qs[128*40], Ks[128*40], Vt[16*136], Ps[128*136];
+    __shared__ u16 Qs[128*40], Ks[128*40], Vt[16*136], Ps[128*136];
     __shared__ float csr[128], linv[128];
     int tid = threadIdx.x, bid = blockIdx.x;
     int h = bid & 127, n = (bid >> 7) & 3, b = bid >> 9;
@@ -501,21 +526,19 @@
         *(uint4*)&Qs[i*40 + 16 + seg] = make_uint4(0,0,0,0);
         *(uint4*)&Ks[i*40 + 16 + seg] = make_uint4(0,0,0,0);
     }
-    for (int vi = tid; vi < 512; vi += 256) {
-        int i = vi >> 2, d4 = (vi & 3)*4;
-        float4 q = *(const float4*)&qr[rowoff + i*16 + d4];
-        float4 k = *(const float4*)&kr[rowoff + i*16 + d4];
-        *(uint2*)&Qs[i*40 + d4] = make_uint2(pk2(q.x,q.y), pk2(q.z,q.w));
-        *(uint2*)&Ks[i*40 + d4] = make_uint2(pk2(k.x,k.y), pk2(k.z,k.w));
-    }
     {
-        int jp = tid >> 2, d4 = (tid & 3)*4;
-        float4 a = *(const float4*)&vhb[vbase + (size_t)(2*jp)*2048 + d4];
-        float4 c = *(const float4*)&vhb[vbase + (size_t)(2*jp+1)*2048 + d4];
-        *(unsigned*)&Vt[(d4+0)*136 + 2*jp] = pk2(a.x, c.x);
-        *(unsigned*)&Vt[(d4+1)*136 + 2*jp] = pk2(a.y, c.y);
-        *(unsigned*)&Vt[(d4+2)*136 + 2*jp] = pk2(a.z, c.z);
-        *(unsigned*)&Vt[(d4+3)*136 + 2*jp] = pk2(a.w, c.w);
+        int i = tid >> 1, half = tid & 1;
+        *(uint4*)&Qs[i*40 + half*8] = *(const uint4*)&qr[rowoff + i*16 + half*8];
+        *(uint4*)&Ks[i*40 + half*8] = *(const uint4*)&kr[rowoff + i*16 + half*8];
+    }
+    {
+        int jp = tid >> 2, q4 = tid & 3;
+        U2 a, c;
+        a.v = *(const uint2*)&vhb[vbase + (size_t)(2*jp)*2048 + q4*4];
+        c.v = *(const uint2*)&vhb[vbase + (size_t)(2*jp+1)*2048 + q4*4];
+        #pragma unroll
+        for (int u = 0; u < 4; ++u)
+            *(unsigned*)&Vt[(q4*4+u)*136 + 2*jp] = (unsigned)a.s[u] | ((unsigned)c.s[u] << 16);
     }
     if (tid < 128) csr[tid] = dacs[((b*128+h)*4+n)*128 + tid];
     __syncthreads();
@@ -565,36 +588,42 @@
     }
     size_t lpb = (size_t)bn*262144 + (size_t)h*2048;
     size_t oab = (size_t)b*1048576 + (size_t)h*8192 + n*16;
+    bool evn = !(lm & 1);
     #pragma unroll
     for (int r = 0; r < 4; ++r) {
         int i0 = r0+quad*4+r, i1 = r1+quad*4+r;
         float o2a = acc0[r]*linv[i0];
         float o2b = acc1[r]*linv[i1];
-        float o1a = o1b[vbase + (size_t)i0*2048 + lm];
-        float o1c = o1b[vbase + (size_t)i1*2048 + lm];
+        float o1a = bf2f(o1b[vbase + (size_t)i0*2048 + lm]);
+        float o1c = bf2f(o1b[vbase + (size_t)i1*2048 + lm]);
         float la  = lepe[lpb + (size_t)i0*16 + lm];
         float lc  = lepe[lpb + (size_t)i1*16 + lm];
-        attn[oab + (size_t)i0*64 + lm] = 0.5f*(o1a + o2a) + la;
-        attn[oab + (size_t)i1*64 + lm] = 0.5f*(o1c + o2b) + lc;
+        unsigned ua = f2bf(0.5f*(o1a + o2a) + la);
+        unsigned uc = f2bf(0.5f*(o1c + o2b) + lc);
+        unsigned upa = (unsigned)__shfl_xor((int)ua,1,64);
+        unsigned upc = (unsigned)__shfl_xor((int)uc,1,64);
+        if (evn) {
+            *(unsigned*)&attn[oab + (size_t)i0*64 + lm] = (ua & 0xffff) | (upa << 16);
+            *(unsigned*)&attn[oab + (size_t)i1*64 + lm] = (uc & 0xffff) | (upc << 16);
+        }
     }
 }
 
 __global__ __launch_bounds__(256) void k_proj_ln(
-    const float* __restrict__ attn, const float* __restrict__ x,
+    const u16* __restrict__ attn, const float* __restrict__ x,
     const float* __restrict__ ow, const float* __restrict__ ob,
     const float* __restrict__ g1, const float* __restrict__ b1,
-    float* __restrict__ t1)
+    u16* __restrict__ t1)
 {
-    __shared__ unsigned short As[128*72];
-    __shared__ unsigned short Bs[64*72];
+    __shared__ u16 As[128*72];
+    __shared__ u16 Bs[64*72];
     __shared__ float XT[8704];
     int tid = threadIdx.x, bid = blockIdx.x;
     int pbase = bid*128;
     int b = pbase >> 14, p0 = pbase & 16383;
-    for (int vi = tid; vi < 2048; vi += 256) {
-        int p = vi >> 4, c4 = (vi & 15)*4;
-        float4 v = *(const float4*)&attn[((size_t)(pbase+p))*64 + c4];
-        *(uint2*)&As[p*72 + c4] = make_uint2(pk2(v.x,v.y), pk2(v.z,v.w));
+    for (int vi = tid; vi < 1024; vi += 256) {
+        int p = vi >> 3, seg = (vi & 7)*8;
+        *(uint4*)&As[p*72 + seg] = *(const uint4*)&attn[((size_t)(pbase+p))*64 + seg];
     }
     for (int vi = tid; vi < 512; vi += 256) {
         int kp = vi >> 4, c4 = (vi & 15)*4;
@@ -682,32 +711,34 @@
             for (int nt = 0; nt < 4; ++nt)
                 outT[(M0+mt*16+quad*4+r)*68 + nt*16 + lm] = res[mt][nt][r];
     __syncthreads();
-    for (int vi = tid; vi < 2048; vi += 256) {
-        int p = vi >> 4, c4 = (vi & 15)*4;
-        *(float4*)&t1[((size_t)(pbase+p))*64 + c4] = *(const float4*)&outT[p*68 + c4];
+    for (int vi = tid; vi < 1024; vi += 256) {
+        int p = vi >> 3, seg = (vi & 7)*8;
+        float4 f0 = *(const float4*)&outT[p*68 + seg];
+        float4 f1 = *(const float4*)&outT[p*68 + seg + 4];
+        uint4 o = make_uint4(pk2(f0.x,f0.y), pk2(f0.z,f0.w), pk2(f1.x,f1.y), pk2(f1.z,f1.w));
+        *(uint4*)&t1[((size_t)(pbase+p))*64 + seg] = o;
     }
 }
 
 __global__ __launch_bounds__(256) void k_ffn(
-    const float* __restrict__ t1, const float* __restrict__ w1,
+    const u16* __restrict__ t1, const float* __restrict__ w1,
     const float* __restrict__ b1f, const float* __restrict__ w2,
     const float* __restrict__ b2f, const float* __restrict__ g2,
     const float* __restrict__ bb2, float* __restrict__ outp)
 {
-    __shared__ unsigned short At1[128*72];
-    __shared__ unsigned short WH[2*64*72 + 128*72];
+    __shared__ u16 At1[128*72];
+    __shared__ u16 WH[2*64*72 + 128*72];
     __shared__ float sb1[256];
     __shared__ float sb2[64], sg[64], sbb[64];
-    unsigned short* W1b = WH;
-    unsigned short* W2b = WH + 4608;
-    unsigned short* Hid = WH + 9216;
+    u16* W1b = WH;
+    u16* W2b = WH + 4608;
+    u16* Hid = WH + 9216;
     int tid = threadIdx.x, bid = blockIdx.x;
     int pbase = bid*128;
     int b = pbase >> 14, p0 = pbase & 16383;
-    for (int vi = tid; vi < 2048; vi += 256) {
-        int p = vi >> 4, c4 = (vi & 15)*4;
-        float4 v = *(const float4*)&t1[((size_t)(pbase+p))*64 + c4];
-        *(uint2*)&At1[p*72 + c4] = make_uint2(pk2(v.x,v.y), pk2(v.z,v.w));
+    for (int vi = tid; vi < 1024; vi += 256) {
+        int p = vi >> 3, seg = (vi & 7)*8;
+        *(uint4*)&At1[p*72 + seg] = *(const uint4*)&t1[((size_t)(pbase+p))*64 + seg];
     }
     if (tid < 256) sb1[tid] = b1f[tid];
     if (tid < 64) { sb2[tid] = b2f[tid]; sg[tid] = g2[tid]; sbb[tid] = bb2[tid]; }
@@ -876,21 +907,21 @@
 
     const size_t SZ = 4194304;
     float* ws    = (float*)d_ws;
-    float* fused = ws + 0*SZ;
-    float* qrb   = ws + 1*SZ;
-    float* krb   = ws + 2*SZ;
-    float* v5b   = ws + 3*SZ;
+    u16* fused = (u16*)(ws + 0*SZ);
+    u16* qrb   = (u16*)(ws + 1*SZ);
+    u16* krb   = (u16*)(ws + 2*SZ);
+    u16* v5b   = (u16*)(ws + 3*SZ);
     float* lepeb = ws + 4*SZ;
-    float* vhb   = ws + 5*SZ;
-    float* o1b   = ws + 6*SZ;
-    float* attnb = ws + 7*SZ;
-    float* t1b   = ws + 8*SZ;
+    u16* vhb   = (u16*)(ws + 5*SZ);
+    u16* o1b   = (u16*)(ws + 6*SZ);
+    u16* attnb = (u16*)(ws + 7*SZ);
+    u16* t1b   = (u16*)(ws + 8*SZ);
     float* dacs  = ws + 9*SZ;
     float* dbcs  = ws + 9*SZ + 262144;
 
     k_fuse<<<1024, 256, 0, stream>>>(y, th, dw1_w, dw1_b, dw2_w, dw2_b, fused);
-    k_qkv<<<1024, 256, 0, stream>>>(x, fused, qw, qb, kw, kb, vw, vb,
-                                    dt_w, dt_bias, A_log, qrb, krb, v5b, dacs, dbcs);
+    k_qkv<<<512, 256, 0, stream>>>(x, fused, qw, qb, kw, kb, vw, vb,
+                                   dt_w, dt_bias, A_log, qrb, krb, v5b, dacs, dbcs);
     k_cumsum<<<1024, 256, 0, stream>>>(dacs, dbcs);
     k_lepe<<<512, 256, 0, stream>>>(v5b, lepe_w, lepe_b, lepeb);
     k_attn_w1<<<2048, 256, 0, stream>>>(qrb, krb, v5b, dacs, fused);
```

New measurement: 330.6 us. 6.7% less time.
